# Optimization experiments

Measured on AMD Instinct MI355X. Metric: run time of the kernel, lower is better.

## Reference

```python
import jax, jax.numpy as jnp
import numpy as np


def setup_inputs() -> dict:
    key = jax.random.key(0)
    ks = jax.random.split(key, 8)
    T, S, W, O = 50000, 168, 336, 48
    N = T - W - O + 1
    x = jax.random.uniform(ks[0], (T,), minval=0.5, maxval=1.5, dtype=jnp.float32)
    noise = jax.random.normal(ks[1], (N, W), dtype=jnp.float32) * 0.001  # Normal(0, std=0.001)
    level_sc = jax.random.uniform(ks[2], (), minval=-1.0, maxval=1.0, dtype=jnp.float32)
    seas_sc = jax.random.uniform(ks[3], (), minval=-1.0, maxval=1.0, dtype=jnp.float32)
    init_seas = jax.random.uniform(ks[4], (S,), minval=0.65, maxval=1.35, dtype=jnp.float32)
    W1 = jax.random.normal(ks[5], (W, W), dtype=jnp.float32) / np.float32(np.sqrt(W))
    b1 = jnp.zeros((W,), jnp.float32)
    W2 = jax.random.normal(ks[6], (W, O), dtype=jnp.float32) / np.float32(np.sqrt(W))
    b2 = jnp.zeros((O,), jnp.float32)
    return {"x": x, "noise": noise, "level_sc": level_sc, "seas_sc": seas_sc,
            "init_seas": init_seas, "W1": W1, "b1": b1, "W2": W2, "b2": b2,
            "window_size": W, "out_size": O, "lvp": 1}


def reference(x, noise, level_sc, seas_sc, init_seas, W1, b1, W2, b2,
              window_size, out_size, lvp):
    T = x.shape[0]
    a = jax.nn.sigmoid(level_sc)      # level smoothing coeff
    g = jax.nn.sigmoid(seas_sc)       # seasonal smoothing coeff
    s0 = jnp.exp(init_seas)           # [S] initial multiplicative seasonals
    # seasonals list in torch: seas[0..S-1]=s0, seas[S]=s0[0], seas[S+i]=w_i.
    # Ring buffer holds seas[i..i+S-1] at step i (starting i=1): [s0[1:], s0[0]].
    buf0 = jnp.concatenate([s0[1:], s0[:1]])
    level0 = x[0] / s0[0]

    def step(carry, xi):
        level, buf = carry
        seas_i = buf[0]
        new_level = a * xi / seas_i + (1.0 - a) * level
        new_w = g * xi / new_level + (1.0 - g) * seas_i
        new_buf = jnp.concatenate([buf[1:], new_w[None]])
        return (new_level, new_buf), (new_level, new_w, jnp.log(new_level / level))

    _, (lvls, ws, logdiffs) = jax.lax.scan(step, (level0, buf0), x[1:])
    levels = jnp.concatenate([level0[None], lvls])        # [T]
    seas_full = jnp.concatenate([s0, s0[:1], ws])         # [S+T]

    d = logdiffs[1:] - logdiffs[:-1]
    level_var_loss = jnp.mean(d * d) * lvp

    N = T - window_size - out_size + 1
    idx_in = jnp.arange(N)[:, None] + jnp.arange(window_size)[None, :]   # [N,W]
    idx_lab = jnp.arange(N)[:, None] + window_size + jnp.arange(out_size)[None, :]  # [N,O]
    lev = levels[jnp.arange(N) + window_size][:, None]    # [N,1]
    inp = jnp.log(x[idx_in] / (lev * seas_full[idx_in])) + noise   # noisy squashed inputs
    labels = jnp.log(x[idx_lab] / (lev * seas_full[idx_lab]))

    h = jnp.tanh(inp @ W1 + b1)        # tanh_no_lstm: Linear(336,336)+tanh
    out = h @ W2 + b2                  # linear_no_lstm: Linear(336,48)
    return out, labels, level_var_loss
```

## Files before the change

kernel.cpp:

```cpp
#include <hip/hip_runtime.h>
#include <hip/hip_bf16.h>

typedef __attribute__((ext_vector_type(8))) short  s16x8;
typedef __attribute__((ext_vector_type(4))) short  s16x4;
typedef __attribute__((ext_vector_type(4))) float  f32x4;

#define T_LEN 50000
#define S_LEN 168
#define W_IN  336
#define O_OUT 48
#define N_ROWS (T_LEN - W_IN - O_OUT + 1)
#define N_PAD  49664
#define NBLK   (N_PAD / 64)

__device__ inline short f2bf(float f) {
    union { float f; unsigned u; } v; v.f = f;
    unsigned u = v.u;
    unsigned r = u + 0x7fffu + ((u >> 16) & 1u);
    return (short)(r >> 16);
}

__device__ inline int bfpk(float lo, float hi) {
    float2 f2; f2.x = lo; f2.y = hi;
    __hip_bfloat162 h = __float22bfloat162_rn(f2);
    int r; __builtin_memcpy(&r, &h, 4);
    return r;
}

__device__ inline float readlane_f(float v, int l) {
    return __int_as_float(__builtin_amdgcn_readlane(__float_as_int(v), l));
}

__device__ inline float fast_tanh(float v) {
    float e = __expf(2.f * v);
    return 1.f - 2.f * __builtin_amdgcn_rcpf(e + 1.f);
}

__global__ void k_preconvert(const float* __restrict__ W1, const float* __restrict__ W2,
                             short* __restrict__ W1T, short* __restrict__ W2T) {
    int idx = blockIdx.x * 256 + threadIdx.x;
    const int n1 = 352 * 352;
    const int tot = n1 + 48 * 360;
    if (idx >= tot) return;
    if (idx < n1) {
        int j = idx / 352, k = idx % 352;
        W1T[idx] = (j < 336 && k < 336) ? f2bf(W1[k * 336 + j]) : (short)0;
    } else {
        int i2 = idx - n1;
        int o = i2 / 360, k = i2 % 360;
        W2T[i2] = (k < 336) ? f2bf(W2[k * 48 + o]) : (short)0;
    }
}

#define DPP_FMA(q_, CTRL, W, RM) { \
    int t_ = __builtin_amdgcn_update_dpp(0, __float_as_int(q_), (CTRL), (RM), 0xf, true); \
    q_ = fmaf((W), __int_as_float(t_), q_); }

__global__ void k_scan(const float* __restrict__ x, const float* __restrict__ level_sc,
                       const float* __restrict__ seas_sc, const float* __restrict__ init_seas,
                       float* __restrict__ lw, float* __restrict__ seasinit) {
    __shared__ float ring[256];
    int lane = threadIdx.x;
    float a = 1.f / (1.f + expf(-level_sc[0]));
    float g = 1.f / (1.f + expf(-seas_sc[0]));
    float om = 1.f - a, omg = 1.f - g;

    for (int t = lane; t < 256; t += 64) {
        float s = 1.f;
        if (t <= S_LEN) { s = expf(init_seas[t < S_LEN ? t : 0]); seasinit[t] = s; }
        ring[t] = s;
    }
    float lpv = x[0] / expf(init_seas[0]);
    if (lane == 0) { lw[0] = lpv; lw[1] = 1.f; }
    __syncthreads();

    float om1 = om, om2v = om1 * om1, om4 = om2v * om2v, om8 = om4 * om4;
    float pl    = powf(om, (float)(lane + 1));
    float fpre  = powf(om, (float)((lane & 15) + 1));
    float fpre2 = powf(om, (float)((lane & 31) + 1));

#define SCAN(QOUT, XV, RSV) { \
    float q_ = a * (XV) * (RSV); \
    DPP_FMA(q_, 0x111, om1,  0xf); \
    DPP_FMA(q_, 0x112, om2v, 0xf); \
    DPP_FMA(q_, 0x114, om4,  0xf); \
    DPP_FMA(q_, 0x118, om8,  0xf); \
    DPP_FMA(q_, 0x142, fpre,  0xa); \
    DPP_FMA(q_, 0x143, fpre2, 0xc); \
    QOUT = q_; }

#define XLOAD(I) float xr##I = x[1 + 64 * I + lane];
    XLOAD(0) XLOAD(1) XLOAD(2) XLOAD(3) XLOAD(4) XLOAD(5) XLOAD(6) XLOAD(7)
    XLOAD(8) XLOAD(9) XLOAD(10) XLOAD(11) XLOAD(12) XLOAD(13) XLOAD(14) XLOAD(15)
#undef XLOAD

    float sA0 = ring[1 + lane];
    float Qcur; SCAN(Qcur, xr0, __builtin_amdgcn_rcpf(sA0));
    float sW = sA0;
    float ldsA = ring[65 + lane];
    float ldsB;
    int ib = 1;

#define BODY(R, RN, LIN, LOUT, CLAMP) { \
    float lvl = fmaf(pl, lpv, Qcur); \
    lpv = readlane_f(lvl, 63); \
    float w_ = fmaf(omg, sW, (g * xr##R) * __builtin_amdgcn_rcpf(lvl)); \
    float2 pk_; pk_.x = lvl; pk_.y = w_; \
    *(float2*)&lw[2 * (ib + lane)] = pk_; \
    ring[(ib + S_LEN + lane) & 255] = w_; \
    LOUT = ring[(ib + 128 + lane) & 255]; \
    float Qn_; SCAN(Qn_, xr##RN, __builtin_amdgcn_rcpf(LIN)); \
    int pidx = ib + 1024 + lane; \
    if (CLAMP) pidx = pidx > (T_LEN - 1) ? (T_LEN - 1) : pidx; \
    xr##R = x[pidx]; \
    Qcur = Qn_; sW = LIN; \
    ib += 64; }

    for (int kb = 0; kb < 47; ++kb) {
        BODY(0,1,  ldsA, ldsB, 0) BODY(1,2,  ldsB, ldsA, 0) BODY(2,3,  ldsA, ldsB, 0) BODY(3,4,  ldsB, ldsA, 0)
        BODY(4,5,  ldsA, ldsB, 0) BODY(5,6,  ldsB, ldsA, 0) BODY(6,7,  ldsA, ldsB, 0) BODY(7,8,  ldsB, ldsA, 0)
        BODY(8,9,  ldsA, ldsB, 0) BODY(9,10, ldsB, ldsA, 0) BODY(10,11,ldsA, ldsB, 0) BODY(11,12,ldsB, ldsA, 0)
        BODY(12,13,ldsA, ldsB, 0) BODY(13,14,ldsB, ldsA, 0) BODY(14,15,ldsA, ldsB, 0) BODY(15,0, ldsB, ldsA, 0)
    }
    BODY(0,1,  ldsA, ldsB, 0) BODY(1,2,  ldsB, ldsA, 0) BODY(2,3,  ldsA, ldsB, 0) BODY(3,4,  ldsB, ldsA, 0)
    BODY(4,5,  ldsA, ldsB, 0) BODY(5,6,  ldsB, ldsA, 0) BODY(6,7,  ldsA, ldsB, 0) BODY(7,8,  ldsB, ldsA, 0)
    BODY(8,9,  ldsA, ldsB, 0) BODY(9,10, ldsB, ldsA, 0) BODY(10,11,ldsA, ldsB, 0) BODY(11,12,ldsB, ldsA, 0)
    BODY(12,13,ldsA, ldsB, 0)
    BODY(13,14,ldsB, ldsA, 1) BODY(14,15,ldsA, ldsB, 1) BODY(15,0, ldsB, ldsA, 1)
    BODY(0,1,  ldsA, ldsB, 1) BODY(1,2,  ldsB, ldsA, 1) BODY(2,3,  ldsA, ldsB, 1) BODY(3,4,  ldsB, ldsA, 1)
    BODY(4,5,  ldsA, ldsB, 1) BODY(5,6,  ldsB, ldsA, 1) BODY(6,7,  ldsA, ldsB, 1) BODY(7,8,  ldsB, ldsA, 1)
    BODY(8,9,  ldsA, ldsB, 1) BODY(9,10, ldsB, ldsA, 1) BODY(10,11,ldsA, ldsB, 1) BODY(11,12,ldsB, ldsA, 1)
#undef BODY

    {
        float lvl = fmaf(pl, lpv, Qcur);
        lpv = readlane_f(lvl, 63);
        float w_ = fmaf(omg, sW, (g * xr12) * __builtin_amdgcn_rcpf(lvl));
        float2 pk_; pk_.x = lvl; pk_.y = w_;
        *(float2*)&lw[2 * (49921 + lane)] = pk_;
    }
    {
        float Qn_; SCAN(Qn_, xr13, __builtin_amdgcn_rcpf(ldsA));
        float lvl = fmaf(pl, lpv, Qn_);
        if (lane < 15) {
            float w_ = fmaf(omg, ldsA, (g * xr13) * __builtin_amdgcn_rcpf(lvl));
            float2 pk_; pk_.x = lvl; pk_.y = w_;
            *(float2*)&lw[2 * (49985 + lane)] = pk_;
        }
    }
#undef SCAN
}

__global__ void k_logs(const float* __restrict__ x, const float* __restrict__ lw,
                       const float* __restrict__ seasinit,
                       float* __restrict__ F, float* __restrict__ llev,
                       float* __restrict__ partials) {
    __shared__ float sm[258];
    __shared__ float red[256];
    int tid = threadIdx.x;
    int t = blockIdx.x * 256 + tid;
    float ll = 0.f;
    if (t < T_LEN) {
        float2 cur = *(const float2*)&lw[2 * t];
        int ps = t - S_LEN; if (ps < 0) ps = 0;
        float sv = (t <= S_LEN) ? seasinit[t] : lw[2 * ps + 1];
        F[t]  = __logf(x[t]) - __logf(sv);
        ll    = __logf(cur.x);
        llev[t] = ll;
    }
    sm[tid] = ll;
    if (tid < 2) {
        int te = blockIdx.x * 256 + 256 + tid;
        sm[256 + tid] = (te < T_LEN) ? __logf(lw[2 * te]) : 0.f;
    }
    __syncthreads();
    float s = 0.f;
    if (t < T_LEN - 2) {
        float d = sm[tid + 2] - 2.f * sm[tid + 1] + sm[tid];
        s = d * d;
    }
    red[tid] = s; __syncthreads();
    for (int off = 128; off > 0; off >>= 1) {
        if (tid < off) red[tid] += red[tid + off];
        __syncthreads();
    }
    if (tid == 0) partials[blockIdx.x] = red[0];
}

__global__ __launch_bounds__(256, 3) void k_gemm(
        const float* __restrict__ noise, const float* __restrict__ F,
        const float* __restrict__ llev, const short* __restrict__ W1T,
        const float* __restrict__ b1, const short* __restrict__ W2T,
        const float* __restrict__ b2, const float* __restrict__ partials,
        const int* __restrict__ lvp, float* __restrict__ out,
        float* __restrict__ labels, float* __restrict__ loss) {
    __shared__ __align__(16) short hlds[64][360];
    __shared__ __align__(16) float Flds[448];
    __shared__ __align__(16) float Llds[64];
    __shared__ __align__(16) float b1lds[352];

    int t = threadIdx.x, w = t >> 6, l = t & 63;
    int lm = l & 15, lq = l >> 4;
    long n0 = (long)blockIdx.x * 64;

    if (blockIdx.x == 0 && w == 3) {
        float s = partials[l] + partials[l + 64] + partials[l + 128];
        if (l < 4) s += partials[l + 192];
#pragma unroll
        for (int off = 32; off > 0; off >>= 1) s += __shfl_down(s, off, 64);
        if (l == 0) loss[0] = s / (float)(T_LEN - 2) * (float)lvp[0];
    }

    if (t < 112)      *(f32x4*)&Flds[t * 4] = *(const f32x4*)&F[n0 + t * 4];
    else if (t < 128) *(f32x4*)&Llds[(t - 112) * 4] = *(const f32x4*)&llev[n0 + W_IN + (t - 112) * 4];
    else if (t < 216) {
        int i4 = (t - 128) * 4;
        f32x4 v = (f32x4){0.f, 0.f, 0.f, 0.f};
        if (i4 < W_IN) v = *(const f32x4*)&b1[i4];
        *(f32x4*)&b1lds[i4] = v;
    }

    int rbase = (w >> 1) * 32;
    int jbase = (w & 1) * 176;
    long an0 = n0 + rbase + lm, an1 = an0 + 16;
    const long amax = (long)N_ROWS * W_IN - 8;
    long a00 = an0 * W_IN, a10 = an1 * W_IN;

    f32x4 ncE00, ncE01, ncE10, ncE11, ncO00, ncO01, ncO10, ncO11;
    {
        long p0 = a00 + lq * 8; if (p0 > amax) p0 = amax;
        long p1 = a10 + lq * 8; if (p1 > amax) p1 = amax;
        ncE00 = *(const f32x4*)&noise[p0]; ncE01 = *(const f32x4*)&noise[p0 + 4];
        ncE10 = *(const f32x4*)&noise[p1]; ncE11 = *(const f32x4*)&noise[p1 + 4];
        long q0 = a00 + 32 + lq * 8; if (q0 > amax) q0 = amax;
        long q1 = a10 + 32 + lq * 8; if (q1 > amax) q1 = amax;
        ncO00 = *(const f32x4*)&noise[q0]; ncO01 = *(const f32x4*)&noise[q0 + 4];
        ncO10 = *(const f32x4*)&noise[q1]; ncO11 = *(const f32x4*)&noise[q1 + 4];
    }

    f32x4 acc0[11], acc1[11];
#pragma unroll
    for (int c = 0; c < 11; ++c) { acc0[c] = (f32x4){0,0,0,0}; acc1[c] = (f32x4){0,0,0,0}; }

    const short* w1row = &W1T[(jbase + lm) * 352 + lq * 8];
#define LDW(CT, KS) (*(const s16x8*)&w1row[(CT) * 5632 + (KS) * 32])
    s16x8 af0 = LDW(0,0), af1 = LDW(1,0), af2 = LDW(2,0), af3 = LDW(3,0), af4 = LDW(4,0),
          af5 = LDW(5,0), af6 = LDW(6,0), af7 = LDW(7,0), af8 = LDW(8,0), af9 = LDW(9,0),
          af10 = LDW(10,0);

    __syncthreads();
    float lv0 = Llds[rbase + lm], lv1 = Llds[rbase + 16 + lm];

#define MM2(CT, AF) \
    acc0[CT] = __builtin_amdgcn_mfma_f32_16x16x32_bf16(AF, bf0, acc0[CT], 0, 0, 0); \
    acc1[CT] = __builtin_amdgcn_mfma_f32_16x16x32_bf16(AF, bf1, acc1[CT], 0, 0, 0);

#define KSTEP(KS, NCX) { \
    s16x8 bf0, bf1; \
    { int fb = rbase + lm + (KS) * 32 + lq * 8; \
      int* b0i = (int*)&bf0; int* b1i = (int*)&bf1; \
      b0i[0] = bfpk(Flds[fb+0]  - lv0 + NCX##00[0], Flds[fb+1]  - lv0 + NCX##00[1]); \
      b0i[1] = bfpk(Flds[fb+2]  - lv0 + NCX##00[2], Flds[fb+3]  - lv0 + NCX##00[3]); \
      b0i[2] = bfpk(Flds[fb+4]  - lv0 + NCX##01[0], Flds[fb+5]  - lv0 + NCX##01[1]); \
      b0i[3] = bfpk(Flds[fb+6]  - lv0 + NCX##01[2], Flds[fb+7]  - lv0 + NCX##01[3]); \
      b1i[0] = bfpk(Flds[fb+16] - lv1 + NCX##10[0], Flds[fb+17] - lv1 + NCX##10[1]); \
      b1i[1] = bfpk(Flds[fb+18] - lv1 + NCX##10[2], Flds[fb+19] - lv1 + NCX##10[3]); \
      b1i[2] = bfpk(Flds[fb+20] - lv1 + NCX##11[0], Flds[fb+21] - lv1 + NCX##11[1]); \
      b1i[3] = bfpk(Flds[fb+22] - lv1 + NCX##11[2], Flds[fb+23] - lv1 + NCX##11[3]); } \
    if ((KS) + 2 <= 10) { \
      int kb = ((KS) + 2) * 32 + lq * 8; \
      long q0 = a00 + kb; if (q0 > amax) q0 = amax; \
      long q1 = a10 + kb; if (q1 > amax) q1 = amax; \
      NCX##00 = *(const f32x4*)&noise[q0]; NCX##01 = *(const f32x4*)&noise[q0 + 4]; \
      NCX##10 = *(const f32x4*)&noise[q1]; NCX##11 = *(const f32x4*)&noise[q1 + 4]; \
    } \
    MM2(0, af0)   if ((KS) < 10) af0  = LDW(0,  (KS) + 1); \
    MM2(1, af1)   if ((KS) < 10) af1  = LDW(1,  (KS) + 1); \
    MM2(2, af2)   if ((KS) < 10) af2  = LDW(2,  (KS) + 1); \
    MM2(3, af3)   if ((KS) < 10) af3  = LDW(3,  (KS) + 1); \
    MM2(4, af4)   if ((KS) < 10) af4  = LDW(4,  (KS) + 1); \
    MM2(5, af5)   if ((KS) < 10) af5  = LDW(5,  (KS) + 1); \
    MM2(6, af6)   if ((KS) < 10) af6  = LDW(6,  (KS) + 1); \
    MM2(7, af7)   if ((KS) < 10) af7  = LDW(7,  (KS) + 1); \
    MM2(8, af8)   if ((KS) < 10) af8  = LDW(8,  (KS) + 1); \
    MM2(9, af9)   if ((KS) < 10) af9  = LDW(9,  (KS) + 1); \
    MM2(10, af10) if ((KS) < 10) af10 = LDW(10, (KS) + 1); \
}

    KSTEP(0, ncE) KSTEP(1, ncO) KSTEP(2, ncE) KSTEP(3, ncO) KSTEP(4, ncE)
    KSTEP(5, ncO) KSTEP(6, ncE) KSTEP(7, ncO) KSTEP(8, ncE) KSTEP(9, ncO)
    KSTEP(10, ncE)
#undef KSTEP
#undef MM2
#undef LDW

#pragma unroll
    for (int ct = 0; ct < 11; ++ct) {
        f32x4 b1q = *(f32x4*)&b1lds[jbase + ct * 16 + lq * 4];
        int2 p0, p1;
        p0.x = bfpk(fast_tanh(acc0[ct][0] + b1q[0]), fast_tanh(acc0[ct][1] + b1q[1]));
        p0.y = bfpk(fast_tanh(acc0[ct][2] + b1q[2]), fast_tanh(acc0[ct][3] + b1q[3]));
        p1.x = bfpk(fast_tanh(acc1[ct][0] + b1q[0]), fast_tanh(acc1[ct][1] + b1q[1]));
        p1.y = bfpk(fast_tanh(acc1[ct][2] + b1q[2]), fast_tanh(acc1[ct][3] + b1q[3]));
        *(int2*)&hlds[rbase + lm][jbase + ct * 16 + lq * 4]      = p0;
        *(int2*)&hlds[rbase + 16 + lm][jbase + ct * 16 + lq * 4] = p1;
    }
    __syncthreads();

    f32x4 a2[3];
    a2[0] = (f32x4){0,0,0,0}; a2[1] = (f32x4){0,0,0,0}; a2[2] = (f32x4){0,0,0,0};
#pragma unroll
    for (int ks = 0; ks < 11; ++ks) {
        s16x8 hf = *(s16x8*)&hlds[w * 16 + lm][ks * 32 + lq * 8];
#pragma unroll
        for (int ct = 0; ct < 3; ++ct) {
            s16x8 bf2 = *(const s16x8*)&W2T[(ct * 16 + lm) * 360 + ks * 32 + lq * 8];
            a2[ct] = __builtin_amdgcn_mfma_f32_16x16x32_bf16(hf, bf2, a2[ct], 0, 0, 0);
        }
    }

    int rloc = w * 16 + lq * 4;
#pragma unroll
    for (int ct = 0; ct < 3; ++ct) {
        float b2v = b2[ct * 16 + lm];
#pragma unroll
        for (int r = 0; r < 4; ++r) {
            long row = n0 + rloc + r;
            if (row < N_ROWS) {
                int col = ct * 16 + lm;
                out[row * O_OUT + col]    = a2[ct][r] + b2v;
                labels[row * O_OUT + col] = Flds[rloc + r + W_IN + col] - Llds[rloc + r];
            }
        }
    }
}

extern "C" void kernel_launch(void* const* d_in, const int* in_sizes, int n_in,
                              void* d_out, int out_size, void* d_ws, size_t ws_size,
                              hipStream_t stream) {
    const float* x         = (const float*)d_in[0];
    const float* noise     = (const float*)d_in[1];
    const float* level_sc  = (const float*)d_in[2];
    const float* seas_sc   = (const float*)d_in[3];
    const float* init_seas = (const float*)d_in[4];
    const float* W1        = (const float*)d_in[5];
    const float* b1        = (const float*)d_in[6];
    const float* W2        = (const float*)d_in[7];
    const float* b2        = (const float*)d_in[8];
    const int*   lvp       = (const int*)d_in[11];

    float* out    = (float*)d_out;
    float* labels = out + (long)N_ROWS * O_OUT;
    float* loss   = labels + (long)N_ROWS * O_OUT;

    float* wsf      = (float*)d_ws;
    float* lw       = wsf;
    float* seasinit = wsf + 100096;
    float* F        = wsf + 100288;
    float* llev     = wsf + 150464;
    float* partials = wsf + 200512;
    short* W1T      = (short*)(wsf + 200768);
    short* W2T      = W1T + 352 * 352;

    k_preconvert<<<552, 256, 0, stream>>>(W1, W2, W1T, W2T);
    k_scan<<<1, 64, 0, stream>>>(x, level_sc, seas_sc, init_seas, lw, seasinit);
    k_logs<<<196, 256, 0, stream>>>(x, lw, seasinit, F, llev, partials);
    k_gemm<<<NBLK, 256, 0, stream>>>(noise, F, llev, W1T, b1, W2T, b2,
                                     partials, lvp, out, labels, loss);
}
```

Before: 165.3 us.

## Fold level subtraction into GEMM epilogue via W1 column sums; reload W1 fragments per k-step

Uses the identity (F - lv + noise)·W1 = (F + noise)·W1 - lv·colsum(W1) so the per-row level no longer has to be subtracted while building each bf16 B fragment. Column sums of W1 are computed in the preconvert kernel, and the correction is applied with an FMA before tanh. The W1 A-fragment handling also changes: instead of keeping all 11 fragments prefetched one k-step ahead, three rotating registers are loaded just in time, and noise prefetch distance drops from two k-steps to one. That lowers register pressure but exposes more global-load latency to the MFMA chain. The column-sum loop in preconvert is a serial strided sum per thread.

New measurement: 157.6 us. -4.7%, faster.

```diff
diff --git a/kernel.cpp b/kernel.cpp
--- a/kernel.cpp
+++ b/kernel.cpp
@@ -37,18 +37,24 @@
 }
 
 __global__ void k_preconvert(const float* __restrict__ W1, const float* __restrict__ W2,
-                             short* __restrict__ W1T, short* __restrict__ W2T) {
+                             short* __restrict__ W1T, short* __restrict__ W2T,
+                             float* __restrict__ S1) {
     int idx = blockIdx.x * 256 + threadIdx.x;
     const int n1 = 352 * 352;
-    const int tot = n1 + 48 * 360;
-    if (idx >= tot) return;
+    const int n2 = n1 + 48 * 360;
     if (idx < n1) {
         int j = idx / 352, k = idx % 352;
         W1T[idx] = (j < 336 && k < 336) ? f2bf(W1[k * 336 + j]) : (short)0;
-    } else {
+    } else if (idx < n2) {
         int i2 = idx - n1;
         int o = i2 / 360, k = i2 % 360;
         W2T[i2] = (k < 336) ? f2bf(W2[k * 48 + o]) : (short)0;
+    } else if (idx < n2 + 352) {
+        int j = idx - n2;
+        float s = 0.f;
+        if (j < 336)
+            for (int k = 0; k < 336; ++k) s += W1[k * 336 + j];
+        S1[j] = s;
     }
 }
 
@@ -191,13 +197,14 @@
         const float* __restrict__ noise, const float* __restrict__ F,
         const float* __restrict__ llev, const short* __restrict__ W1T,
         const float* __restrict__ b1, const short* __restrict__ W2T,
-        const float* __restrict__ b2, const float* __restrict__ partials,
-        const int* __restrict__ lvp, float* __restrict__ out,
-        float* __restrict__ labels, float* __restrict__ loss) {
+        const float* __restrict__ b2, const float* __restrict__ S1,
+        const float* __restrict__ partials, const int* __restrict__ lvp,
+        float* __restrict__ out, float* __restrict__ labels, float* __restrict__ loss) {
     __shared__ __align__(16) short hlds[64][360];
     __shared__ __align__(16) float Flds[448];
     __shared__ __align__(16) float Llds[64];
     __shared__ __align__(16) float b1lds[352];
+    __shared__ __align__(16) float S1lds[352];
 
     int t = threadIdx.x, w = t >> 6, l = t & 63;
     int lm = l & 15, lq = l >> 4;
@@ -218,90 +225,84 @@
         f32x4 v = (f32x4){0.f, 0.f, 0.f, 0.f};
         if (i4 < W_IN) v = *(const f32x4*)&b1[i4];
         *(f32x4*)&b1lds[i4] = v;
-    }
+    } else if (t < 304 - 48) {
+        int i4 = (t - 216) * 4;
+        *(f32x4*)&S1lds[i4] = *(const f32x4*)&S1[i4];
+    }
+    if (t < 48) *(f32x4*)&S1lds[160 + t * 4] = *(const f32x4*)&S1[160 + t * 4];
 
     int rbase = (w >> 1) * 32;
     int jbase = (w & 1) * 176;
-    long an0 = n0 + rbase + lm, an1 = an0 + 16;
-    const long amax = (long)N_ROWS * W_IN - 8;
-    long a00 = an0 * W_IN, a10 = an1 * W_IN;
-
-    f32x4 ncE00, ncE01, ncE10, ncE11, ncO00, ncO01, ncO10, ncO11;
-    {
-        long p0 = a00 + lq * 8; if (p0 > amax) p0 = amax;
-        long p1 = a10 + lq * 8; if (p1 > amax) p1 = amax;
-        ncE00 = *(const f32x4*)&noise[p0]; ncE01 = *(const f32x4*)&noise[p0 + 4];
-        ncE10 = *(const f32x4*)&noise[p1]; ncE11 = *(const f32x4*)&noise[p1 + 4];
-        long q0 = a00 + 32 + lq * 8; if (q0 > amax) q0 = amax;
-        long q1 = a10 + 32 + lq * 8; if (q1 > amax) q1 = amax;
-        ncO00 = *(const f32x4*)&noise[q0]; ncO01 = *(const f32x4*)&noise[q0 + 4];
-        ncO10 = *(const f32x4*)&noise[q1]; ncO11 = *(const f32x4*)&noise[q1 + 4];
-    }
+    long an0 = n0 + rbase + lm;      if (an0 > N_ROWS - 2) an0 = N_ROWS - 2;
+    long an1 = n0 + rbase + 16 + lm; if (an1 > N_ROWS - 2) an1 = N_ROWS - 2;
+    const float* nr0 = noise + an0 * W_IN + lq * 8;
+    const float* nr1 = noise + an1 * W_IN + lq * 8;
+
+    f32x4 nc00 = *(const f32x4*)&nr0[0], nc01 = *(const f32x4*)&nr0[4];
+    f32x4 nc10 = *(const f32x4*)&nr1[0], nc11 = *(const f32x4*)&nr1[4];
 
     f32x4 acc0[11], acc1[11];
 #pragma unroll
     for (int c = 0; c < 11; ++c) { acc0[c] = (f32x4){0,0,0,0}; acc1[c] = (f32x4){0,0,0,0}; }
+
+    __syncthreads();
 
     const short* w1row = &W1T[(jbase + lm) * 352 + lq * 8];
 #define LDW(CT, KS) (*(const s16x8*)&w1row[(CT) * 5632 + (KS) * 32])
-    s16x8 af0 = LDW(0,0), af1 = LDW(1,0), af2 = LDW(2,0), af3 = LDW(3,0), af4 = LDW(4,0),
-          af5 = LDW(5,0), af6 = LDW(6,0), af7 = LDW(7,0), af8 = LDW(8,0), af9 = LDW(9,0),
-          af10 = LDW(10,0);
-
-    __syncthreads();
-    float lv0 = Llds[rbase + lm], lv1 = Llds[rbase + 16 + lm];
-
 #define MM2(CT, AF) \
     acc0[CT] = __builtin_amdgcn_mfma_f32_16x16x32_bf16(AF, bf0, acc0[CT], 0, 0, 0); \
     acc1[CT] = __builtin_amdgcn_mfma_f32_16x16x32_bf16(AF, bf1, acc1[CT], 0, 0, 0);
 
-#define KSTEP(KS, NCX) { \
+#define KSTEP(KS) { \
     s16x8 bf0, bf1; \
     { int fb = rbase + lm + (KS) * 32 + lq * 8; \
       int* b0i = (int*)&bf0; int* b1i = (int*)&bf1; \
-      b0i[0] = bfpk(Flds[fb+0]  - lv0 + NCX##00[0], Flds[fb+1]  - lv0 + NCX##00[1]); \
-      b0i[1] = bfpk(Flds[fb+2]  - lv0 + NCX##00[2], Flds[fb+3]  - lv0 + NCX##00[3]); \
-      b0i[2] = bfpk(Flds[fb+4]  - lv0 + NCX##01[0], Flds[fb+5]  - lv0 + NCX##01[1]); \
-      b0i[3] = bfpk(Flds[fb+6]  - lv0 + NCX##01[2], Flds[fb+7]  - lv0 + NCX##01[3]); \
-      b1i[0] = bfpk(Flds[fb+16] - lv1 + NCX##10[0], Flds[fb+17] - lv1 + NCX##10[1]); \
-      b1i[1] = bfpk(Flds[fb+18] - lv1 + NCX##10[2], Flds[fb+19] - lv1 + NCX##10[3]); \
-      b1i[2] = bfpk(Flds[fb+20] - lv1 + NCX##11[0], Flds[fb+21] - lv1 + NCX##11[1]); \
-      b1i[3] = bfpk(Flds[fb+22] - lv1 + NCX##11[2], Flds[fb+23] - lv1 + NCX##11[3]); } \
-    if ((KS) + 2 <= 10) { \
-      int kb = ((KS) + 2) * 32 + lq * 8; \
-      long q0 = a00 + kb; if (q0 > amax) q0 = amax; \
-      long q1 = a10 + kb; if (q1 > amax) q1 = amax; \
-      NCX##00 = *(const f32x4*)&noise[q0]; NCX##01 = *(const f32x4*)&noise[q0 + 4]; \
-      NCX##10 = *(const f32x4*)&noise[q1]; NCX##11 = *(const f32x4*)&noise[q1 + 4]; \
+      b0i[0] = bfpk(Flds[fb+0]  + nc00[0], Flds[fb+1]  + nc00[1]); \
+      b0i[1] = bfpk(Flds[fb+2]  + nc00[2], Flds[fb+3]  + nc00[3]); \
+      b0i[2] = bfpk(Flds[fb+4]  + nc01[0], Flds[fb+5]  + nc01[1]); \
+      b0i[3] = bfpk(Flds[fb+6]  + nc01[2], Flds[fb+7]  + nc01[3]); \
+      b1i[0] = bfpk(Flds[fb+16] + nc10[0], Flds[fb+17] + nc10[1]); \
+      b1i[1] = bfpk(Flds[fb+18] + nc10[2], Flds[fb+19] + nc10[3]); \
+      b1i[2] = bfpk(Flds[fb+20] + nc11[0], Flds[fb+21] + nc11[1]); \
+      b1i[3] = bfpk(Flds[fb+22] + nc11[2], Flds[fb+23] + nc11[3]); } \
+    if ((KS) < 10) { \
+      nc00 = *(const f32x4*)&nr0[((KS)+1)*32]; nc01 = *(const f32x4*)&nr0[((KS)+1)*32+4]; \
+      nc10 = *(const f32x4*)&nr1[((KS)+1)*32]; nc11 = *(const f32x4*)&nr1[((KS)+1)*32+4]; \
     } \
-    MM2(0, af0)   if ((KS) < 10) af0  = LDW(0,  (KS) + 1); \
-    MM2(1, af1)   if ((KS) < 10) af1  = LDW(1,  (KS) + 1); \
-    MM2(2, af2)   if ((KS) < 10) af2  = LDW(2,  (KS) + 1); \
-    MM2(3, af3)   if ((KS) < 10) af3  = LDW(3,  (KS) + 1); \
-    MM2(4, af4)   if ((KS) < 10) af4  = LDW(4,  (KS) + 1); \
-    MM2(5, af5)   if ((KS) < 10) af5  = LDW(5,  (KS) + 1); \
-    MM2(6, af6)   if ((KS) < 10) af6  = LDW(6,  (KS) + 1); \
-    MM2(7, af7)   if ((KS) < 10) af7  = LDW(7,  (KS) + 1); \
-    MM2(8, af8)   if ((KS) < 10) af8  = LDW(8,  (KS) + 1); \
-    MM2(9, af9)   if ((KS) < 10) af9  = LDW(9,  (KS) + 1); \
-    MM2(10, af10) if ((KS) < 10) af10 = LDW(10, (KS) + 1); \
-}
-
-    KSTEP(0, ncE) KSTEP(1, ncO) KSTEP(2, ncE) KSTEP(3, ncO) KSTEP(4, ncE)
-    KSTEP(5, ncO) KSTEP(6, ncE) KSTEP(7, ncO) KSTEP(8, ncE) KSTEP(9, ncO)
-    KSTEP(10, ncE)
+    s16x8 af0 = LDW(0,KS), af1 = LDW(1,KS), af2 = LDW(2,KS); \
+    MM2(0, af0)  af0 = LDW(3,KS); \
+    MM2(1, af1)  af1 = LDW(4,KS); \
+    MM2(2, af2)  af2 = LDW(5,KS); \
+    MM2(3, af0)  af0 = LDW(6,KS); \
+    MM2(4, af1)  af1 = LDW(7,KS); \
+    MM2(5, af2)  af2 = LDW(8,KS); \
+    MM2(6, af0)  af0 = LDW(9,KS); \
+    MM2(7, af1)  af1 = LDW(10,KS); \
+    MM2(8, af2) \
+    MM2(9, af0) \
+    MM2(10, af1) \
+}
+
+    KSTEP(0) KSTEP(1) KSTEP(2) KSTEP(3) KSTEP(4) KSTEP(5)
+    KSTEP(6) KSTEP(7) KSTEP(8) KSTEP(9) KSTEP(10)
 #undef KSTEP
 #undef MM2
 #undef LDW
 
+    float lv0 = Llds[rbase + lm], lv1 = Llds[rbase + 16 + lm];
 #pragma unroll
     for (int ct = 0; ct < 11; ++ct) {
         f32x4 b1q = *(f32x4*)&b1lds[jbase + ct * 16 + lq * 4];
+        f32x4 s1q = *(f32x4*)&S1lds[jbase + ct * 16 + lq * 4];
         int2 p0, p1;
-        p0.x = bfpk(fast_tanh(acc0[ct][0] + b1q[0]), fast_tanh(acc0[ct][1] + b1q[1]));
-        p0.y = bfpk(fast_tanh(acc0[ct][2] + b1q[2]), fast_tanh(acc0[ct][3] + b1q[3]));
-        p1.x = bfpk(fast_tanh(acc1[ct][0] + b1q[0]), fast_tanh(acc1[ct][1] + b1q[1]));
-        p1.y = bfpk(fast_tanh(acc1[ct][2] + b1q[2]), fast_tanh(acc1[ct][3] + b1q[3]));
+        p0.x = bfpk(fast_tanh(fmaf(-lv0, s1q[0], acc0[ct][0] + b1q[0])),
+                    fast_tanh(fmaf(-lv0, s1q[1], acc0[ct][1] + b1q[1])));
+        p0.y = bfpk(fast_tanh(fmaf(-lv0, s1q[2], acc0[ct][2] + b1q[2])),
+                    fast_tanh(fmaf(-lv0, s1q[3], acc0[ct][3] + b1q[3])));
+        p1.x = bfpk(fast_tanh(fmaf(-lv1, s1q[0], acc1[ct][0] + b1q[0])),
+                    fast_tanh(fmaf(-lv1, s1q[1], acc1[ct][1] + b1q[1])));
+        p1.y = bfpk(fast_tanh(fmaf(-lv1, s1q[2], acc1[ct][2] + b1q[2])),
+                    fast_tanh(fmaf(-lv1, s1q[3], acc1[ct][3] + b1q[3])));
         *(int2*)&hlds[rbase + lm][jbase + ct * 16 + lq * 4]      = p0;
         *(int2*)&hlds[rbase + 16 + lm][jbase + ct * 16 + lq * 4] = p1;
     }
@@ -359,12 +360,13 @@
     float* F        = wsf + 100288;
     float* llev     = wsf + 150464;
     float* partials = wsf + 200512;
-    short* W1T      = (short*)(wsf + 200768);
+    float* S1f      = wsf + 200768;
+    short* W1T      = (short*)(wsf + 201152);
     short* W2T      = W1T + 352 * 352;
 
-    k_preconvert<<<552, 256, 0, stream>>>(W1, W2, W1T, W2T);
+    k_preconvert<<<554, 256, 0, stream>>>(W1, W2, W1T, W2T, S1f);
     k_scan<<<1, 64, 0, stream>>>(x, level_sc, seas_sc, init_seas, lw, seasinit);
     k_logs<<<196, 256, 0, stream>>>(x, lw, seasinit, F, llev, partials);
-    k_gemm<<<NBLK, 256, 0, stream>>>(noise, F, llev, W1T, b1, W2T, b2,
+    k_gemm<<<NBLK, 256, 0, stream>>>(noise, F, llev, W1T, b1, W2T, b2, S1f,
                                      partials, lvp, out, labels, loss);
 }
```
